# Kernel tuning notes

Hardware: AMD Instinct MI355X
Metric: run time of the kernel (lower is better)

Reference implementation:

```python
import jax, jax.numpy as jnp
import numpy as np
import math

NUM_CONVS = 4
GN_GROUPS = 32
GN_EPS = 1e-5
FPN_STRIDES = (8, 16, 32, 64, 128)
PRIOR_PROB = 0.01


def conv3x3(x, w, b):
    # x: [N,C,H,W], w: [O,I,3,3]
    y = jax.lax.conv_general_dilated(
        x, w, window_strides=(1, 1), padding='SAME',
        dimension_numbers=('NCHW', 'OIHW', 'NCHW'))
    return y + b[None, :, None, None]


def group_norm(x, gamma, beta):
    n, c, h, w = x.shape
    xg = x.reshape(n, GN_GROUPS, c // GN_GROUPS, h, w)
    mean = xg.mean(axis=(2, 3, 4), keepdims=True)
    var = xg.var(axis=(2, 3, 4), keepdims=True)
    xn = ((xg - mean) * jax.lax.rsqrt(var + GN_EPS)).reshape(n, c, h, w)
    return xn * gamma[None, :, None, None] + beta[None, :, None, None]


def subnet(x, ws, bs, gws, gbs):
    # NUM_CONVS x (conv3x3 -> GN -> ReLU)
    for i in range(NUM_CONVS):
        x = jax.nn.relu(group_norm(conv3x3(x, ws[i], bs[i]), gws[i], gbs[i]))
    return x


def permute_to_N_HWA_K(x, k):
    n = x.shape[0]
    return x.transpose(0, 2, 3, 1).reshape(n, -1, k)


def setup_inputs() -> dict:
    key = jax.random.key(0)
    ks = jax.random.split(key, 16)
    C, K = 256, 80
    feats = {
        'p3': jax.random.normal(ks[0], (1, C, 80, 80), jnp.float32),
        'p4': jax.random.normal(ks[1], (1, C, 40, 40), jnp.float32),
        'p5': jax.random.normal(ks[2], (1, C, 20, 20), jnp.float32),
        'p6': jax.random.normal(ks[3], (1, C, 10, 10), jnp.float32),
        'p7': jax.random.normal(ks[4], (1, C, 5, 5), jnp.float32),
    }
    std = 0.01
    bias_value = -math.log((1 - PRIOR_PROB) / PRIOR_PROB)
    params = {
        'cls_w': std * jax.random.normal(ks[5], (NUM_CONVS, C, C, 3, 3), jnp.float32),
        'cls_b': jnp.zeros((NUM_CONVS, C), jnp.float32),
        'cls_gn_w': jnp.ones((NUM_CONVS, C), jnp.float32),
        'cls_gn_b': jnp.zeros((NUM_CONVS, C), jnp.float32),
        'box_w': std * jax.random.normal(ks[6], (NUM_CONVS, C, C, 3, 3), jnp.float32),
        'box_b': jnp.zeros((NUM_CONVS, C), jnp.float32),
        'box_gn_w': jnp.ones((NUM_CONVS, C), jnp.float32),
        'box_gn_b': jnp.zeros((NUM_CONVS, C), jnp.float32),
        'score_w': std * jax.random.normal(ks[7], (K, C, 3, 3), jnp.float32),
        'score_b': jnp.full((K,), bias_value, jnp.float32),
        'pred_w': std * jax.random.normal(ks[8], (4, C, 3, 3), jnp.float32),
        'pred_b': jnp.zeros((4,), jnp.float32),
        'iou_w': std * jax.random.normal(ks[9], (1, C, 3, 3), jnp.float32),
        'iou_b': jnp.zeros((1,), jnp.float32),
        'scales': jnp.ones((5,), jnp.float32),
    }
    return {**feats, **params}


def reference(p3, p4, p5, p6, p7,
              cls_w, cls_b, cls_gn_w, cls_gn_b,
              box_w, box_b, box_gn_w, box_gn_b,
              score_w, score_b, pred_w, pred_b, iou_w, iou_b, scales):
    features = [p3, p4, p5, p6, p7]
    logits, bbox_reg, ious = [], [], []
    for l, feat in enumerate(features):
        c = subnet(feat, cls_w, cls_b, cls_gn_w, cls_gn_b)
        b = subnet(feat, box_w, box_b, box_gn_w, box_gn_b)
        logit = conv3x3(c, score_w, score_b)          # [N,80,H,W]
        iou = conv3x3(b, iou_w, iou_b)                # [N,1,H,W]
        bp = conv3x3(b, pred_w, pred_b) * scales[l]   # Scale module
        # norm_reg_targets=True branch
        reg = jax.nn.relu(bp) * FPN_STRIDES[l]        # [N,4,H,W]
        logits.append(permute_to_N_HWA_K(logit, 80))
        bbox_reg.append(permute_to_N_HWA_K(reg, 4))
        ious.append(permute_to_N_HWA_K(iou, 1))
    box_cls = jnp.concatenate(logits, axis=1)    # [N, sumHW, 80]
    box_delta = jnp.concatenate(bbox_reg, axis=1)  # [N, sumHW, 4]
    box_iou = jnp.concatenate(ious, axis=1)      # [N, sumHW, 1]
    # pack into one array for a single output: [N, sumHW, 85]
    return jnp.concatenate([box_cls, box_delta, box_iou], axis=-1)
```

## Files before the change

### kernel.cpp

```cpp
#include <hip/hip_runtime.h>

typedef unsigned short u16;
typedef __attribute__((ext_vector_type(8))) short bf16x8;
typedef __attribute__((ext_vector_type(4))) float f32x4;

#define NLEV 5
#define CCH 256
#define KTOT 2304
#define P_TOT 8525
#define PP_TOT 9165

__constant__ int   c_HW[NLEV]     = {6400, 1600, 400, 100, 25};
__constant__ int   c_W[NLEV]      = {80, 40, 20, 10, 5};
__constant__ int   c_off[NLEV]    = {0, 6400, 8000, 8400, 8500};
__constant__ int   c_poff[NLEV]   = {0, 6724, 8488, 8972, 9116};
__constant__ int   c_pts[NLEV+1]  = {0, 100, 125, 132, 134, 135};
__constant__ float c_stridef[NLEV]= {8.f, 16.f, 32.f, 64.f, 128.f};

__device__ __forceinline__ u16 f2bf(float f){
  union { float f; unsigned u; } v; v.f = f;
  unsigned r = v.u + 0x7fffu + ((v.u >> 16) & 1u);
  return (u16)(r >> 16);
}

__device__ __forceinline__ void g2l16(const u16* g, u16* l, int lane){
#if defined(__has_builtin)
#if __has_builtin(__builtin_amdgcn_global_load_lds)
  __builtin_amdgcn_global_load_lds(
      (const __attribute__((address_space(1))) unsigned int*)g,
      (__attribute__((address_space(3))) unsigned int*)l, 16, 0, 0);
  return;
#endif
#endif
  *(uint4*)(l + lane*8) = *(const uint4*)g;
}

template<int MODE>
__global__ __launch_bounds__(256) void gemm_conv(
    const u16* __restrict__ Xc, const u16* __restrict__ Xb,
    const u16* __restrict__ Wc, const u16* __restrict__ Wb,
    const float* __restrict__ bc, const float* __restrict__ bb,
    float* __restrict__ Yc, float* __restrict__ Yb,
    float* __restrict__ stats,
    const float* __restrict__ predb, const float* __restrict__ ioub,
    const float* __restrict__ scales, float* __restrict__ out)
{
  __shared__ u16 sA[128*32];
  __shared__ u16 sB[64*32];
  __shared__ float sstat[16][2];

  const int ptile = blockIdx.x, mtile = blockIdx.y, z = blockIdx.z;
  int lv = 0;
  #pragma unroll
  for (int i = 1; i < NLEV; i++) if (ptile >= c_pts[i]) lv = i;
  const int ptl = ptile - c_pts[lv];
  const int HW = c_HW[lv], Wl = c_W[lv];
  const int tid = threadIdx.x, wv = tid >> 6, ln = tid & 63;
  const int quad = ln >> 4, l15 = ln & 15;

  const u16* X  = z ? Xb : Xc;
  const u16* WA = z ? Wb : Wc;

  const int kl   = (ln & 3) * 8;
  const int rsub = ln >> 2;

  const u16* asrc0 = WA + (size_t)(mtile*128 + wv*32 + rsub) * KTOT + kl;
  const u16* asrc1 = asrc0 + (size_t)16 * KTOT;
  u16* adst0 = &sA[(wv*32)      * 32];
  u16* adst1 = &sA[(wv*32 + 16) * 32];

  const int prow = wv*16 + rsub;
  const int p = ptl*64 + prow;
  int pbase = 0;
  if (p < HW) { int h = p / Wl; int wi = p - h*Wl; pbase = h*(Wl+2) + wi; }
  const u16* bsrc = X + (size_t)(c_poff[lv] + pbase) * CCH + kl;
  u16* bdst = &sB[(wv*16) * 32];

  const u16* afp[2]; const u16* bfp[4];
  #pragma unroll
  for (int i = 0; i < 2; i++) afp[i] = &sA[((wv*32 + i*16 + l15) << 5) + quad*8];
  #pragma unroll
  for (int i = 0; i < 4; i++) bfp[i] = &sB[((i*16 + l15) << 5) + quad*8];

  f32x4 acc[2][4];
  #pragma unroll
  for (int i = 0; i < 2; i++)
    #pragma unroll
    for (int j = 0; j < 4; j++) acc[i][j] = (f32x4){0.f, 0.f, 0.f, 0.f};

  const int wrow = Wl + 2;
  for (int ch = 0; ch < 72; ch++) {
    const int tap = ch >> 3;
    const int dh = tap / 3, dw = tap - dh*3;
    const int aoff = ch * 32;
    const int boff = (dh*wrow + dw)*CCH + ((ch & 7) << 5);
    g2l16(asrc0 + aoff, adst0, ln);
    g2l16(asrc1 + aoff, adst1, ln);
    g2l16(bsrc + boff, bdst, ln);
    __syncthreads();
    bf16x8 af[2], bfr[4];
    #pragma unroll
    for (int i = 0; i < 2; i++) af[i]  = *(const bf16x8*)afp[i];
    #pragma unroll
    for (int i = 0; i < 4; i++) bfr[i] = *(const bf16x8*)bfp[i];
    #pragma unroll
    for (int i = 0; i < 2; i++)
      #pragma unroll
      for (int j = 0; j < 4; j++)
        acc[i][j] = __builtin_amdgcn_mfma_f32_16x16x32_bf16(af[i], bfr[j], acc[i][j], 0, 0, 0);
    __syncthreads();
  }

  const int nrem = HW - ptl*64;
  if (MODE == 0) {
    if (tid < 32) sstat[tid >> 1][tid & 1] = 0.f;
    __syncthreads();
    const float* bias = z ? bb : bc;
    float* Y = z ? Yb : Yc;
    #pragma unroll
    for (int mi = 0; mi < 2; mi++) {
      const int m0 = mtile*128 + wv*32 + mi*16 + quad*4;
      float s = 0.f, sq = 0.f;
      #pragma unroll
      for (int ni = 0; ni < 4; ni++) {
        const int nl = ni*16 + l15;
        f32x4 v = acc[mi][ni];
        #pragma unroll
        for (int r = 0; r < 4; r++) v[r] += bias[m0 + r];
        if (nl < nrem) {
          const size_t n = (size_t)(c_off[lv] + ptl*64 + nl);
          *(f32x4*)&Y[n*CCH + m0] = v;
          #pragma unroll
          for (int r = 0; r < 4; r++) { s += v[r]; sq += v[r]*v[r]; }
        }
      }
      #pragma unroll
      for (int o = 1; o < 16; o <<= 1) { s += __shfl_xor(s, o); sq += __shfl_xor(sq, o); }
      if (l15 == 0) {
        const int g = (wv*32 + mi*16 + quad*4) >> 3;
        atomicAdd(&sstat[g][0], s);
        atomicAdd(&sstat[g][1], sq);
      }
    }
    __syncthreads();
    if (tid < 32) {
      const int g = tid >> 1, c = tid & 1;
      atomicAdd(&stats[(((size_t)z*NLEV + lv)*32 + mtile*16 + g)*2 + c], sstat[g][c]);
    }
  } else {
    const float scl = scales[lv];
    const float stf = c_stridef[lv];
    #pragma unroll
    for (int mi = 0; mi < 2; mi++) {
      const int m0 = wv*32 + mi*16 + quad*4;
      if (m0 >= 85) continue;
      #pragma unroll
      for (int ni = 0; ni < 4; ni++) {
        const int nl = ni*16 + l15;
        if (nl >= nrem) continue;
        const size_t n = (size_t)(c_off[lv] + ptl*64 + nl);
        f32x4 v = acc[mi][ni];
        #pragma unroll
        for (int r = 0; r < 4; r++) {
          const int m = m0 + r;
          const float val = v[r];
          if (z == 0) {
            if (m < 80) out[n*85 + m] = val + bc[m];
          } else {
            if (m < 4) {
              const float t = (val + predb[m]) * scl;
              out[n*85 + 80 + m] = fmaxf(t, 0.f) * stf;
            } else if (m == 4) {
              out[n*85 + 84] = val + ioub[0];
            }
          }
        }
      }
    }
  }
}

__global__ __launch_bounds__(256) void gn_relu(
    const float* __restrict__ Yc, const float* __restrict__ Yb,
    const float* __restrict__ stats,
    const float* __restrict__ gwc, const float* __restrict__ gbc,
    const float* __restrict__ gwb, const float* __restrict__ gbb,
    u16* __restrict__ Xc, u16* __restrict__ Xb)
{
  const int t = blockIdx.x * 256 + threadIdx.x;
  if (t >= 2 * P_TOT * 32) return;
  const int br = t / (P_TOT * 32);
  const int r  = t - br * (P_TOT * 32);
  const int pg = r >> 5;
  const int c0 = (r & 31) << 3;
  int lv = 0;
  #pragma unroll
  for (int i = 1; i < NLEV; i++) if (pg >= c_off[i]) lv = i;
  const int pl = pg - c_off[lv];
  const int Wl = c_W[lv];
  const int g = c0 >> 3;
  const float* st = &stats[(((size_t)br*NLEV + lv)*32 + g)*2];
  const float cnt = 8.f * (float)c_HW[lv];
  const float mean = st[0] / cnt;
  const float var  = st[1] / cnt - mean*mean;
  const float rstd = rsqrtf(var + 1e-5f);
  const float* Y  = br ? Yb : Yc;
  const float* gw = br ? gwb : gwc;
  const float* gb = br ? gbb : gbc;
  u16* X = br ? Xb : Xc;
  const float* y = &Y[(size_t)pg*CCH + c0];
  const int h = pl / Wl, wi = pl - h*Wl;
  const size_t pidx = (size_t)(c_poff[lv] + (h+1)*(Wl+2) + (wi+1));
  union { u16 u[8]; uint4 v; } pk;
  #pragma unroll
  for (int i = 0; i < 8; i++) {
    const float v = (y[i] - mean)*rstd*gw[c0+i] + gb[c0+i];
    pk.u[i] = f2bf(fmaxf(v, 0.f));
  }
  *(uint4*)&X[pidx*CCH + c0] = pk.v;
}

__global__ __launch_bounds__(256) void feat2bf(
    const float* __restrict__ p3, const float* __restrict__ p4,
    const float* __restrict__ p5, const float* __restrict__ p6,
    const float* __restrict__ p7, u16* __restrict__ X)
{
  const int t = blockIdx.x * 256 + threadIdx.x;
  if (t >= P_TOT * 32) return;
  const int pg = t >> 5, c0 = (t & 31) << 3;
  int lv = 0;
  #pragma unroll
  for (int i = 1; i < NLEV; i++) if (pg >= c_off[i]) lv = i;
  const int pl = pg - c_off[lv];
  const float* src = lv==0 ? p3 : lv==1 ? p4 : lv==2 ? p5 : lv==3 ? p6 : p7;
  const int HW = c_HW[lv], Wl = c_W[lv];
  const int h = pl / Wl, wi = pl - h*Wl;
  const size_t pidx = (size_t)(c_poff[lv] + (h+1)*(Wl+2) + (wi+1));
  union { u16 u[8]; uint4 v; } pk;
  #pragma unroll
  for (int i = 0; i < 8; i++)
    pk.u[i] = f2bf(src[(size_t)(c0+i)*HW + pl]);
  *(uint4*)&X[pidx*CCH + c0] = pk.v;
}

__global__ __launch_bounds__(256) void wconv(
    const float* __restrict__ cw, const float* __restrict__ bw,
    u16* __restrict__ Wc, u16* __restrict__ Wb)
{
  const size_t N = (size_t)4*256*KTOT;
  const size_t t = (size_t)blockIdx.x * 256 + threadIdx.x;
  if (t >= 2*N) return;
  const float* src = (t < N) ? cw : bw;
  u16* dst = (t < N) ? Wc : Wb;
  const size_t i = (t < N) ? t : t - N;
  const size_t lc = i / KTOT;
  const int kk = (int)(i - lc*KTOT);
  const int tap = kk >> 8, ci = kk & 255;
  dst[i] = f2bf(src[(lc*256 + ci)*9 + tap]);
}

__global__ __launch_bounds__(256) void hconv(
    const float* __restrict__ sw, const float* __restrict__ pw,
    const float* __restrict__ iw, u16* __restrict__ Whc, u16* __restrict__ Whb)
{
  const int N = 128 * KTOT;
  const int t = blockIdx.x * 256 + threadIdx.x;
  if (t >= 2*N) return;
  const int i = (t < N) ? t : t - N;
  const int co = i / KTOT, kk = i - co*KTOT;
  const int tap = kk >> 8, ci = kk & 255;
  float v = 0.f;
  if (t < N) {
    if (co < 80) v = sw[(co*256 + ci)*9 + tap];
    Whc[i] = f2bf(v);
  } else {
    if (co < 4)       v = pw[(co*256 + ci)*9 + tap];
    else if (co == 4) v = iw[ci*9 + tap];
    Whb[i] = f2bf(v);
  }
}

extern "C" void kernel_launch(void* const* d_in, const int* in_sizes, int n_in,
                              void* d_out, int out_size, void* d_ws, size_t ws_size,
                              hipStream_t stream)
{
  const float* p3      = (const float*)d_in[0];
  const float* p4      = (const float*)d_in[1];
  const float* p5      = (const float*)d_in[2];
  const float* p6      = (const float*)d_in[3];
  const float* p7      = (const float*)d_in[4];
  const float* cls_w   = (const float*)d_in[5];
  const float* cls_b   = (const float*)d_in[6];
  const float* cls_gw  = (const float*)d_in[7];
  const float* cls_gb  = (const float*)d_in[8];
  const float* box_w   = (const float*)d_in[9];
  const float* box_b   = (const float*)d_in[10];
  const float* box_gw  = (const float*)d_in[11];
  const float* box_gb  = (const float*)d_in[12];
  const float* score_w = (const float*)d_in[13];
  const float* score_b = (const float*)d_in[14];
  const float* pred_w  = (const float*)d_in[15];
  const float* pred_b  = (const float*)d_in[16];
  const float* iou_w   = (const float*)d_in[17];
  const float* iou_b   = (const float*)d_in[18];
  const float* scales  = (const float*)d_in[19];
  float* out = (float*)d_out;

  char* w = (char*)d_ws;
  size_t o = 0;
  auto alloc = [&](size_t b) { void* p = w + o; o += (b + 255) & ~(size_t)255; return p; };
  u16* WRC = (u16*)alloc((size_t)4*256*KTOT*2);
  u16* WRB = (u16*)alloc((size_t)4*256*KTOT*2);
  u16* WHC = (u16*)alloc((size_t)128*KTOT*2);
  u16* WHB = (u16*)alloc((size_t)128*KTOT*2);
  u16* XF  = (u16*)alloc((size_t)PP_TOT*CCH*2);
  u16* XC0 = (u16*)alloc((size_t)PP_TOT*CCH*2);
  u16* XC1 = (u16*)alloc((size_t)PP_TOT*CCH*2);
  u16* XB0 = (u16*)alloc((size_t)PP_TOT*CCH*2);
  u16* XB1 = (u16*)alloc((size_t)PP_TOT*CCH*2);
  float* YC = (float*)alloc((size_t)P_TOT*CCH*4);
  float* YB = (float*)alloc((size_t)P_TOT*CCH*4);
  float* ST = (float*)alloc((size_t)2*5*32*2*4);

  hipMemsetAsync(XF, 0, (size_t)5*PP_TOT*CCH*2, stream);
  hipMemsetAsync(ST, 0, (size_t)2*5*32*2*4, stream);

  wconv<<<dim3((unsigned)(((size_t)2*4*256*KTOT + 255)/256)), 256, 0, stream>>>(cls_w, box_w, WRC, WRB);
  hconv<<<dim3((2*128*KTOT + 255)/256), 256, 0, stream>>>(score_w, pred_w, iou_w, WHC, WHB);
  feat2bf<<<dim3((P_TOT*32 + 255)/256), 256, 0, stream>>>(p3, p4, p5, p6, p7, XF);

  const u16* xci = XF; const u16* xbi = XF;
  u16* xcs[4] = {XC0, XC1, XC0, XC1};
  u16* xbs[4] = {XB0, XB1, XB0, XB1};
  for (int l = 0; l < 4; l++) {
    gemm_conv<0><<<dim3(135, 2, 2), 256, 0, stream>>>(
        xci, xbi, WRC + (size_t)l*256*KTOT, WRB + (size_t)l*256*KTOT,
        cls_b + l*256, box_b + l*256, YC, YB, ST,
        nullptr, nullptr, nullptr, nullptr);
    gn_relu<<<dim3((2*P_TOT*32 + 255)/256), 256, 0, stream>>>(
        YC, YB, ST, cls_gw + l*256, cls_gb + l*256, box_gw + l*256, box_gb + l*256,
        xcs[l], xbs[l]);
    if (l < 3) hipMemsetAsync(ST, 0, (size_t)2*5*32*2*4, stream);
    xci = xcs[l]; xbi = xbs[l];
  }
  gemm_conv<1><<<dim3(135, 1, 2), 256, 0, stream>>>(
      xci, xbi, WHC, WHB, score_b, nullptr, nullptr, nullptr, nullptr,
      pred_b, iou_b, scales, out);
}
```

Baseline: 408.4 us.

## Split conv GEMM K across blocks with 64-wide swizzled LDS tiles and separate GN stats

Each conv GEMM now splits the 2304-long K dimension into two halves across extra grid z-slices. Each slice writes its own fp32 partial output buffer. The K step per iteration grows from 32 to 64, with an XOR swizzle on LDS rows to avoid bank conflicts. Bias addition and GroupNorm statistics move out of the GEMM epilogue into a new gn_stats kernel that sums the partials, and the head epilogue moves into a head_out kernel. The goal is more blocks in flight and fewer barriers per K element, paid for by extra partial-buffer traffic and more kernel launches per layer.

Measured after the change: 452.3 us. 1.11x slower.

```diff
diff --git a/kernel.cpp b/kernel.cpp
--- a/kernel.cpp
+++ b/kernel.cpp
@@ -36,51 +36,43 @@
 }
 
 template<int MODE>
-__global__ __launch_bounds__(256) void gemm_conv(
+__global__ __launch_bounds__(256, 4) void gemm_conv(
     const u16* __restrict__ Xc, const u16* __restrict__ Xb,
     const u16* __restrict__ Wc, const u16* __restrict__ Wb,
-    const float* __restrict__ bc, const float* __restrict__ bb,
-    float* __restrict__ Yc, float* __restrict__ Yb,
-    float* __restrict__ stats,
-    const float* __restrict__ predb, const float* __restrict__ ioub,
-    const float* __restrict__ scales, float* __restrict__ out)
-{
-  __shared__ u16 sA[128*32];
-  __shared__ u16 sB[64*32];
-  __shared__ float sstat[16][2];
-
-  const int ptile = blockIdx.x, mtile = blockIdx.y, z = blockIdx.z;
+    float* __restrict__ Y0c, float* __restrict__ Y1c,
+    float* __restrict__ Y0b, float* __restrict__ Y1b,
+    float* __restrict__ OP)
+{
+  __shared__ u16 sA[128*64];
+  __shared__ u16 sB[64*64];
+
+  const int ptile = blockIdx.x, mtile = blockIdx.y;
+  const int kh = blockIdx.z >> 1, br = blockIdx.z & 1;
   int lv = 0;
   #pragma unroll
   for (int i = 1; i < NLEV; i++) if (ptile >= c_pts[i]) lv = i;
   const int ptl = ptile - c_pts[lv];
-  const int HW = c_HW[lv], Wl = c_W[lv];
+  const int HW = c_HW[lv], Wl = c_W[lv], wrow = Wl + 2;
   const int tid = threadIdx.x, wv = tid >> 6, ln = tid & 63;
   const int quad = ln >> 4, l15 = ln & 15;
-
-  const u16* X  = z ? Xb : Xc;
-  const u16* WA = z ? Wb : Wc;
-
-  const int kl   = (ln & 3) * 8;
-  const int rsub = ln >> 2;
-
-  const u16* asrc0 = WA + (size_t)(mtile*128 + wv*32 + rsub) * KTOT + kl;
-  const u16* asrc1 = asrc0 + (size_t)16 * KTOT;
-  u16* adst0 = &sA[(wv*32)      * 32];
-  u16* adst1 = &sA[(wv*32 + 16) * 32];
-
-  const int prow = wv*16 + rsub;
-  const int p = ptl*64 + prow;
-  int pbase = 0;
-  if (p < HW) { int h = p / Wl; int wi = p - h*Wl; pbase = h*(Wl+2) + wi; }
-  const u16* bsrc = X + (size_t)(c_poff[lv] + pbase) * CCH + kl;
-  u16* bdst = &sB[(wv*16) * 32];
-
-  const u16* afp[2]; const u16* bfp[4];
-  #pragma unroll
-  for (int i = 0; i < 2; i++) afp[i] = &sA[((wv*32 + i*16 + l15) << 5) + quad*8];
-  #pragma unroll
-  for (int i = 0; i < 4; i++) bfp[i] = &sB[((i*16 + l15) << 5) + quad*8];
+  const int lr = ln >> 3;
+  const int gsw = (ln & 7) ^ lr;
+
+  const u16* X  = br ? Xb : Xc;
+  const u16* WA = br ? Wb : Wc;
+
+  const u16* abase = WA + (size_t)(mtile*128 + wv*32 + lr) * KTOT + gsw*8;
+  u16* adst = &sA[(wv*32) * 64];
+
+  const u16* bptr[2];
+  #pragma unroll
+  for (int j = 0; j < 2; j++) {
+    const int p = ptl*64 + wv*16 + j*8 + lr;
+    int pb = 0;
+    if (p < HW) { int h = p / Wl; int wi = p - h*Wl; pb = h*wrow + wi; }
+    bptr[j] = X + (size_t)(c_poff[lv] + pb) * CCH + gsw*8;
+  }
+  u16* bdst = &sB[(wv*16) * 64];
 
   f32x4 acc[2][4];
   #pragma unroll
@@ -88,101 +80,112 @@
     #pragma unroll
     for (int j = 0; j < 4; j++) acc[i][j] = (f32x4){0.f, 0.f, 0.f, 0.f};
 
-  const int wrow = Wl + 2;
-  for (int ch = 0; ch < 72; ch++) {
-    const int tap = ch >> 3;
+  const int s0 = kh * 18, s1 = s0 + 18;
+  for (int s = s0; s < s1; s++) {
+    const int tap = s >> 2;
     const int dh = tap / 3, dw = tap - dh*3;
-    const int aoff = ch * 32;
-    const int boff = (dh*wrow + dw)*CCH + ((ch & 7) << 5);
-    g2l16(asrc0 + aoff, adst0, ln);
-    g2l16(asrc1 + aoff, adst1, ln);
-    g2l16(bsrc + boff, bdst, ln);
+    const u16* as = abase + (size_t)s * 64;
+    g2l16(as,            adst,         ln);
+    g2l16(as +  8*KTOT,  adst +  8*64, ln);
+    g2l16(as + 16*KTOT,  adst + 16*64, ln);
+    g2l16(as + 24*KTOT,  adst + 24*64, ln);
+    const int bsh = (dh*wrow + dw)*CCH + ((s & 3) << 6);
+    g2l16(bptr[0] + bsh, bdst,         ln);
+    g2l16(bptr[1] + bsh, bdst +  8*64, ln);
     __syncthreads();
-    bf16x8 af[2], bfr[4];
-    #pragma unroll
-    for (int i = 0; i < 2; i++) af[i]  = *(const bf16x8*)afp[i];
-    #pragma unroll
-    for (int i = 0; i < 4; i++) bfr[i] = *(const bf16x8*)bfp[i];
-    #pragma unroll
-    for (int i = 0; i < 2; i++)
+    bf16x8 af[2][2], bf[2][4];
+    #pragma unroll
+    for (int sub = 0; sub < 2; sub++) {
+      const int gbase = (sub*4 + quad) ^ (l15 & 7);
+      #pragma unroll
+      for (int i = 0; i < 2; i++)
+        af[sub][i] = *(const bf16x8*)&sA[(wv*32 + i*16 + l15)*64 + gbase*8];
       #pragma unroll
       for (int j = 0; j < 4; j++)
-        acc[i][j] = __builtin_amdgcn_mfma_f32_16x16x32_bf16(af[i], bfr[j], acc[i][j], 0, 0, 0);
+        bf[sub][j] = *(const bf16x8*)&sB[(j*16 + l15)*64 + gbase*8];
+    }
+    #pragma unroll
+    for (int sub = 0; sub < 2; sub++)
+      #pragma unroll
+      for (int i = 0; i < 2; i++)
+        #pragma unroll
+        for (int j = 0; j < 4; j++)
+          acc[i][j] = __builtin_amdgcn_mfma_f32_16x16x32_bf16(af[sub][i], bf[sub][j], acc[i][j], 0, 0, 0);
     __syncthreads();
   }
 
   const int nrem = HW - ptl*64;
   if (MODE == 0) {
-    if (tid < 32) sstat[tid >> 1][tid & 1] = 0.f;
-    __syncthreads();
-    const float* bias = z ? bb : bc;
-    float* Y = z ? Yb : Yc;
+    float* Y = br ? (kh ? Y1b : Y0b) : (kh ? Y1c : Y0c);
     #pragma unroll
     for (int mi = 0; mi < 2; mi++) {
       const int m0 = mtile*128 + wv*32 + mi*16 + quad*4;
-      float s = 0.f, sq = 0.f;
       #pragma unroll
       for (int ni = 0; ni < 4; ni++) {
         const int nl = ni*16 + l15;
-        f32x4 v = acc[mi][ni];
-        #pragma unroll
-        for (int r = 0; r < 4; r++) v[r] += bias[m0 + r];
         if (nl < nrem) {
           const size_t n = (size_t)(c_off[lv] + ptl*64 + nl);
-          *(f32x4*)&Y[n*CCH + m0] = v;
-          #pragma unroll
-          for (int r = 0; r < 4; r++) { s += v[r]; sq += v[r]*v[r]; }
-        }
-      }
-      #pragma unroll
-      for (int o = 1; o < 16; o <<= 1) { s += __shfl_xor(s, o); sq += __shfl_xor(sq, o); }
-      if (l15 == 0) {
-        const int g = (wv*32 + mi*16 + quad*4) >> 3;
-        atomicAdd(&sstat[g][0], s);
-        atomicAdd(&sstat[g][1], sq);
-      }
-    }
-    __syncthreads();
-    if (tid < 32) {
-      const int g = tid >> 1, c = tid & 1;
-      atomicAdd(&stats[(((size_t)z*NLEV + lv)*32 + mtile*16 + g)*2 + c], sstat[g][c]);
-    }
-  } else {
-    const float scl = scales[lv];
-    const float stf = c_stridef[lv];
-    #pragma unroll
-    for (int mi = 0; mi < 2; mi++) {
-      const int m0 = wv*32 + mi*16 + quad*4;
-      if (m0 >= 85) continue;
-      #pragma unroll
-      for (int ni = 0; ni < 4; ni++) {
-        const int nl = ni*16 + l15;
-        if (nl >= nrem) continue;
-        const size_t n = (size_t)(c_off[lv] + ptl*64 + nl);
-        f32x4 v = acc[mi][ni];
-        #pragma unroll
-        for (int r = 0; r < 4; r++) {
-          const int m = m0 + r;
-          const float val = v[r];
-          if (z == 0) {
-            if (m < 80) out[n*85 + m] = val + bc[m];
-          } else {
-            if (m < 4) {
-              const float t = (val + predb[m]) * scl;
-              out[n*85 + 80 + m] = fmaxf(t, 0.f) * stf;
-            } else if (m == 4) {
-              out[n*85 + 84] = val + ioub[0];
-            }
-          }
+          *(f32x4*)&Y[n*CCH + m0] = acc[mi][ni];
         }
       }
     }
+  } else {
+    float* O = OP + (size_t)(br*2 + kh) * P_TOT * 128;
+    #pragma unroll
+    for (int mi = 0; mi < 2; mi++) {
+      const int m0 = wv*32 + mi*16 + quad*4;
+      #pragma unroll
+      for (int ni = 0; ni < 4; ni++) {
+        const int nl = ni*16 + l15;
+        if (nl < nrem) {
+          const size_t n = (size_t)(c_off[lv] + ptl*64 + nl);
+          *(f32x4*)&O[n*128 + m0] = acc[mi][ni];
+        }
+      }
+    }
+  }
+}
+
+__global__ __launch_bounds__(256) void gn_stats(
+    const float* __restrict__ Y0c, const float* __restrict__ Y1c,
+    const float* __restrict__ Y0b, const float* __restrict__ Y1b,
+    const float* __restrict__ bc, const float* __restrict__ bb,
+    float* __restrict__ stats)
+{
+  const int sl = blockIdx.x, br = blockIdx.y;
+  int lv = 0;
+  #pragma unroll
+  for (int i = 1; i < NLEV; i++) if (sl >= c_pts[i]) lv = i;
+  const int sll = sl - c_pts[lv];
+  const int HW = c_HW[lv];
+  const float* Y0 = br ? Y0b : Y0c;
+  const float* Y1 = br ? Y1b : Y1c;
+  const int c = threadIdx.x;
+  const float b = (br ? bb : bc)[c];
+  float s = 0.f, sq = 0.f;
+  const int p0 = sll * 64;
+  for (int i = 0; i < 64; i++) {
+    const int p = p0 + i;
+    if (p >= HW) break;
+    const size_t idx = (size_t)(c_off[lv] + p) * CCH + c;
+    const float v = Y0[idx] + Y1[idx] + b;
+    s += v; sq += v*v;
+  }
+  s += __shfl_xor(s, 1); sq += __shfl_xor(sq, 1);
+  s += __shfl_xor(s, 2); sq += __shfl_xor(sq, 2);
+  s += __shfl_xor(s, 4); sq += __shfl_xor(sq, 4);
+  if ((c & 7) == 0) {
+    const int g = c >> 3;
+    atomicAdd(&stats[((br*NLEV + lv)*32 + g)*2 + 0], s);
+    atomicAdd(&stats[((br*NLEV + lv)*32 + g)*2 + 1], sq);
   }
 }
 
 __global__ __launch_bounds__(256) void gn_relu(
-    const float* __restrict__ Yc, const float* __restrict__ Yb,
+    const float* __restrict__ Y0c, const float* __restrict__ Y1c,
+    const float* __restrict__ Y0b, const float* __restrict__ Y1b,
     const float* __restrict__ stats,
+    const float* __restrict__ bc, const float* __restrict__ bb,
     const float* __restrict__ gwc, const float* __restrict__ gbc,
     const float* __restrict__ gwb, const float* __restrict__ gbb,
     u16* __restrict__ Xc, u16* __restrict__ Xb)
@@ -204,20 +207,49 @@
   const float mean = st[0] / cnt;
   const float var  = st[1] / cnt - mean*mean;
   const float rstd = rsqrtf(var + 1e-5f);
-  const float* Y  = br ? Yb : Yc;
+  const float* Y0 = br ? Y0b : Y0c;
+  const float* Y1 = br ? Y1b : Y1c;
+  const float* bs = br ? bb : bc;
   const float* gw = br ? gwb : gwc;
   const float* gb = br ? gbb : gbc;
   u16* X = br ? Xb : Xc;
-  const float* y = &Y[(size_t)pg*CCH + c0];
+  const float* y0 = &Y0[(size_t)pg*CCH + c0];
+  const float* y1 = &Y1[(size_t)pg*CCH + c0];
   const int h = pl / Wl, wi = pl - h*Wl;
   const size_t pidx = (size_t)(c_poff[lv] + (h+1)*(Wl+2) + (wi+1));
   union { u16 u[8]; uint4 v; } pk;
   #pragma unroll
   for (int i = 0; i < 8; i++) {
-    const float v = (y[i] - mean)*rstd*gw[c0+i] + gb[c0+i];
+    const float v = (y0[i] + y1[i] + bs[c0+i] - mean)*rstd*gw[c0+i] + gb[c0+i];
     pk.u[i] = f2bf(fmaxf(v, 0.f));
   }
   *(uint4*)&X[pidx*CCH + c0] = pk.v;
+}
+
+__global__ __launch_bounds__(256) void head_out(
+    const float* __restrict__ OP,
+    const float* __restrict__ score_b, const float* __restrict__ pred_b,
+    const float* __restrict__ iou_b, const float* __restrict__ scales,
+    float* __restrict__ out)
+{
+  const int t = blockIdx.x * 256 + threadIdx.x;
+  if (t >= P_TOT * 96) return;
+  const int n = t / 96, m = t - n*96;
+  if (m >= 85) return;
+  int lv = 0;
+  #pragma unroll
+  for (int i = 1; i < NLEV; i++) if (n >= c_off[i]) lv = i;
+  const size_t S = (size_t)P_TOT * 128;
+  const size_t r = (size_t)n * 128;
+  if (m < 80) {
+    out[(size_t)n*85 + m] = OP[r + m] + OP[S + r + m] + score_b[m];
+  } else if (m < 84) {
+    const int mm = m - 80;
+    float v = (OP[2*S + r + mm] + OP[3*S + r + mm] + pred_b[mm]) * scales[lv];
+    out[(size_t)n*85 + 80 + mm] = fmaxf(v, 0.f) * c_stridef[lv];
+  } else {
+    out[(size_t)n*85 + 84] = OP[2*S + r + 4] + OP[3*S + r + 4] + iou_b[0];
+  }
 }
 
 __global__ __launch_bounds__(256) void feat2bf(
@@ -314,36 +346,37 @@
   u16* WHC = (u16*)alloc((size_t)128*KTOT*2);
   u16* WHB = (u16*)alloc((size_t)128*KTOT*2);
   u16* XF  = (u16*)alloc((size_t)PP_TOT*CCH*2);
-  u16* XC0 = (u16*)alloc((size_t)PP_TOT*CCH*2);
-  u16* XC1 = (u16*)alloc((size_t)PP_TOT*CCH*2);
-  u16* XB0 = (u16*)alloc((size_t)PP_TOT*CCH*2);
-  u16* XB1 = (u16*)alloc((size_t)PP_TOT*CCH*2);
-  float* YC = (float*)alloc((size_t)P_TOT*CCH*4);
-  float* YB = (float*)alloc((size_t)P_TOT*CCH*4);
-  float* ST = (float*)alloc((size_t)2*5*32*2*4);
-
-  hipMemsetAsync(XF, 0, (size_t)5*PP_TOT*CCH*2, stream);
-  hipMemsetAsync(ST, 0, (size_t)2*5*32*2*4, stream);
+  u16* XC  = (u16*)alloc((size_t)PP_TOT*CCH*2);
+  u16* XB  = (u16*)alloc((size_t)PP_TOT*CCH*2);
+  float* Y0C = (float*)alloc((size_t)P_TOT*CCH*4);
+  float* Y1C = (float*)alloc((size_t)P_TOT*CCH*4);
+  float* Y0B = (float*)alloc((size_t)P_TOT*CCH*4);
+  float* Y1B = (float*)alloc((size_t)P_TOT*CCH*4);
+  float* OP  = (float*)alloc((size_t)4*P_TOT*128*4);
+  float* ST  = (float*)alloc((size_t)2*NLEV*32*2*4);
+
+  hipMemsetAsync(XF, 0, (size_t)3*PP_TOT*CCH*2, stream);
 
   wconv<<<dim3((unsigned)(((size_t)2*4*256*KTOT + 255)/256)), 256, 0, stream>>>(cls_w, box_w, WRC, WRB);
   hconv<<<dim3((2*128*KTOT + 255)/256), 256, 0, stream>>>(score_w, pred_w, iou_w, WHC, WHB);
   feat2bf<<<dim3((P_TOT*32 + 255)/256), 256, 0, stream>>>(p3, p4, p5, p6, p7, XF);
 
   const u16* xci = XF; const u16* xbi = XF;
-  u16* xcs[4] = {XC0, XC1, XC0, XC1};
-  u16* xbs[4] = {XB0, XB1, XB0, XB1};
   for (int l = 0; l < 4; l++) {
-    gemm_conv<0><<<dim3(135, 2, 2), 256, 0, stream>>>(
+    hipMemsetAsync(ST, 0, (size_t)2*NLEV*32*2*4, stream);
+    gemm_conv<0><<<dim3(135, 2, 4), 256, 0, stream>>>(
         xci, xbi, WRC + (size_t)l*256*KTOT, WRB + (size_t)l*256*KTOT,
-        cls_b + l*256, box_b + l*256, YC, YB, ST,
-        nullptr, nullptr, nullptr, nullptr);
+        Y0C, Y1C, Y0B, Y1B, nullptr);
+    gn_stats<<<dim3(135, 2), 256, 0, stream>>>(
+        Y0C, Y1C, Y0B, Y1B, cls_b + l*256, box_b + l*256, ST);
     gn_relu<<<dim3((2*P_TOT*32 + 255)/256), 256, 0, stream>>>(
-        YC, YB, ST, cls_gw + l*256, cls_gb + l*256, box_gw + l*256, box_gb + l*256,
-        xcs[l], xbs[l]);
-    if (l < 3) hipMemsetAsync(ST, 0, (size_t)2*5*32*2*4, stream);
-    xci = xcs[l]; xbi = xbs[l];
-  }
-  gemm_conv<1><<<dim3(135, 1, 2), 256, 0, stream>>>(
-      xci, xbi, WHC, WHB, score_b, nullptr, nullptr, nullptr, nullptr,
-      pred_b, iou_b, scales, out);
-}
+        Y0C, Y1C, Y0B, Y1B, ST, cls_b + l*256, box_b + l*256,
+        cls_gw + l*256, cls_gb + l*256, box_gw + l*256, box_gb + l*256,
+        XC, XB);
+    xci = XC; xbi = XB;
+  }
+  gemm_conv<1><<<dim3(135, 1, 4), 256, 0, stream>>>(
+      xci, xbi, WHC, WHB, nullptr, nullptr, nullptr, nullptr, OP);
+  head_out<<<dim3((P_TOT*96 + 255)/256), 256, 0, stream>>>(
+      OP, score_b, pred_b, iou_b, scales, out);
+}
```

## Replace LDS-staged conv GEMM with register double-buffered 64x64 wave tiles

Applied to the files above, without the earlier changes.

The implicit-GEMM conv kernel no longer stages A and B tiles through LDS with two barriers per K step. Each wave now loads MFMA fragments straight from global memory into registers, double-buffered across K steps, and computes a 64x64 output tile. For the trunk convs this makes each block cover all 256 output channels, so the grid is halved. The head kernel is remapped so each wave owns one pixel tile and the box branch launches only one channel tile. Activation buffers are single-buffered, and GN stats get a slice per layer that is cleared by one up-front memset instead of memsets between layers. The trade-off is less shared-memory reuse, heavier reliance on L1/L2 for fragment loads, more registers, and fewer resident waves per CU.

Result: slower. 779.1 us (+90.7%).

```diff
diff --git a/kernel.cpp b/kernel.cpp
--- a/kernel.cpp
+++ b/kernel.cpp
@@ -15,24 +15,13 @@
 __constant__ int   c_off[NLEV]    = {0, 6400, 8000, 8400, 8500};
 __constant__ int   c_poff[NLEV]   = {0, 6724, 8488, 8972, 9116};
 __constant__ int   c_pts[NLEV+1]  = {0, 100, 125, 132, 134, 135};
+__constant__ int   c_g4s[NLEV+1]  = {0, 25, 32, 34, 35, 36};
 __constant__ float c_stridef[NLEV]= {8.f, 16.f, 32.f, 64.f, 128.f};
 
 __device__ __forceinline__ u16 f2bf(float f){
   union { float f; unsigned u; } v; v.f = f;
   unsigned r = v.u + 0x7fffu + ((v.u >> 16) & 1u);
   return (u16)(r >> 16);
-}
-
-__device__ __forceinline__ void g2l16(const u16* g, u16* l, int lane){
-#if defined(__has_builtin)
-#if __has_builtin(__builtin_amdgcn_global_load_lds)
-  __builtin_amdgcn_global_load_lds(
-      (const __attribute__((address_space(1))) unsigned int*)g,
-      (__attribute__((address_space(3))) unsigned int*)l, 16, 0, 0);
-  return;
-#endif
-#endif
-  *(uint4*)(l + lane*8) = *(const uint4*)g;
 }
 
 template<int MODE>
@@ -45,91 +34,102 @@
     const float* __restrict__ predb, const float* __restrict__ ioub,
     const float* __restrict__ scales, float* __restrict__ out)
 {
-  __shared__ u16 sA[128*32];
-  __shared__ u16 sB[64*32];
-  __shared__ float sstat[16][2];
-
-  const int ptile = blockIdx.x, mtile = blockIdx.y, z = blockIdx.z;
-  int lv = 0;
-  #pragma unroll
-  for (int i = 1; i < NLEV; i++) if (ptile >= c_pts[i]) lv = i;
-  const int ptl = ptile - c_pts[lv];
-  const int HW = c_HW[lv], Wl = c_W[lv];
+  __shared__ float sstat[32][2];
   const int tid = threadIdx.x, wv = tid >> 6, ln = tid & 63;
   const int quad = ln >> 4, l15 = ln & 15;
 
-  const u16* X  = z ? Xb : Xc;
-  const u16* WA = z ? Wb : Wc;
-
-  const int kl   = (ln & 3) * 8;
-  const int rsub = ln >> 2;
-
-  const u16* asrc0 = WA + (size_t)(mtile*128 + wv*32 + rsub) * KTOT + kl;
-  const u16* asrc1 = asrc0 + (size_t)16 * KTOT;
-  u16* adst0 = &sA[(wv*32)      * 32];
-  u16* adst1 = &sA[(wv*32 + 16) * 32];
-
-  const int prow = wv*16 + rsub;
-  const int p = ptl*64 + prow;
-  int pbase = 0;
-  if (p < HW) { int h = p / Wl; int wi = p - h*Wl; pbase = h*(Wl+2) + wi; }
-  const u16* bsrc = X + (size_t)(c_poff[lv] + pbase) * CCH + kl;
-  u16* bdst = &sB[(wv*16) * 32];
-
-  const u16* afp[2]; const u16* bfp[4];
-  #pragma unroll
-  for (int i = 0; i < 2; i++) afp[i] = &sA[((wv*32 + i*16 + l15) << 5) + quad*8];
-  #pragma unroll
-  for (int i = 0; i < 4; i++) bfp[i] = &sB[((i*16 + l15) << 5) + quad*8];
-
-  f32x4 acc[2][4];
-  #pragma unroll
-  for (int i = 0; i < 2; i++)
+  int lv = 0, ptl, m0, br;
+  if (MODE == 0) {
+    const int ptile = blockIdx.x;
+    br = blockIdx.z;
+    #pragma unroll
+    for (int i = 1; i < NLEV; i++) if (ptile >= c_pts[i]) lv = i;
+    ptl = ptile - c_pts[lv];
+    m0 = wv * 64;
+  } else {
+    const int gx = blockIdx.x, gy = blockIdx.y;
+    br = (gy == 2) ? 1 : 0;
+    m0 = (gy == 1) ? 64 : 0;
+    #pragma unroll
+    for (int i = 1; i < NLEV; i++) if (gx >= c_g4s[i]) lv = i;
+    ptl = (gx - c_g4s[lv]) * 4 + wv;
+    if (ptl >= c_pts[lv+1] - c_pts[lv]) return;
+  }
+  const int HW = c_HW[lv], Wl = c_W[lv], wrow = Wl + 2;
+  const u16* __restrict__ X  = br ? Xb : Xc;
+  const u16* __restrict__ WA = br ? Wb : Wc;
+
+  int ar[4], rb[4];
+  #pragma unroll
+  for (int mt = 0; mt < 4; mt++) ar[mt] = (m0 + mt*16 + l15) * KTOT + quad*8;
+  #pragma unroll
+  for (int nt = 0; nt < 4; nt++) {
+    const int p = ptl*64 + nt*16 + l15;
+    int rbase = wrow + 1;
+    if (p < HW) { const int h = p / Wl, wi = p - h*Wl; rbase = (h+1)*wrow + (wi+1); }
+    rb[nt] = (c_poff[lv] + rbase) * CCH + quad*8;
+  }
+
+  f32x4 acc[4][4];
+  #pragma unroll
+  for (int i = 0; i < 4; i++)
     #pragma unroll
     for (int j = 0; j < 4; j++) acc[i][j] = (f32x4){0.f, 0.f, 0.f, 0.f};
 
-  const int wrow = Wl + 2;
-  for (int ch = 0; ch < 72; ch++) {
-    const int tap = ch >> 3;
-    const int dh = tap / 3, dw = tap - dh*3;
-    const int aoff = ch * 32;
-    const int boff = (dh*wrow + dw)*CCH + ((ch & 7) << 5);
-    g2l16(asrc0 + aoff, adst0, ln);
-    g2l16(asrc1 + aoff, adst1, ln);
-    g2l16(bsrc + boff, bdst, ln);
-    __syncthreads();
-    bf16x8 af[2], bfr[4];
-    #pragma unroll
-    for (int i = 0; i < 2; i++) af[i]  = *(const bf16x8*)afp[i];
-    #pragma unroll
-    for (int i = 0; i < 4; i++) bfr[i] = *(const bf16x8*)bfp[i];
-    #pragma unroll
-    for (int i = 0; i < 2; i++)
-      #pragma unroll
-      for (int j = 0; j < 4; j++)
-        acc[i][j] = __builtin_amdgcn_mfma_f32_16x16x32_bf16(af[i], bfr[j], acc[i][j], 0, 0, 0);
-    __syncthreads();
-  }
+  bf16x8 A0[4], B0[4], A1[4], B1[4];
+
+#define LDFRAG(Af, Bf, S) do {                                              \
+    const int _s = (S);                                                     \
+    const int _tap = _s >> 3;                                               \
+    const int _dh = _tap / 3, _dw = _tap - _dh*3;                           \
+    const int _aof = _s * 32;                                               \
+    const int _bof = ((_dh-1)*wrow + (_dw-1))*CCH + ((_s & 7) << 5);        \
+    _Pragma("unroll")                                                       \
+    for (int _mt = 0; _mt < 4; _mt++)                                       \
+      Af[_mt] = *(const bf16x8*)(WA + ar[_mt] + _aof);                      \
+    _Pragma("unroll")                                                       \
+    for (int _nt = 0; _nt < 4; _nt++)                                       \
+      Bf[_nt] = *(const bf16x8*)(X + rb[_nt] + _bof);                       \
+  } while (0)
+
+#define MFMA16(Af, Bf) do {                                                 \
+    _Pragma("unroll")                                                       \
+    for (int _mt = 0; _mt < 4; _mt++)                                       \
+      _Pragma("unroll")                                                     \
+      for (int _nt = 0; _nt < 4; _nt++)                                     \
+        acc[_mt][_nt] = __builtin_amdgcn_mfma_f32_16x16x32_bf16(            \
+            Af[_mt], Bf[_nt], acc[_mt][_nt], 0, 0, 0);                      \
+  } while (0)
+
+  LDFRAG(A0, B0, 0);
+  for (int s = 0; s < 72; s += 2) {
+    LDFRAG(A1, B1, s + 1);
+    MFMA16(A0, B0);
+    const int s2 = (s + 2 < 72) ? s + 2 : 70;
+    LDFRAG(A0, B0, s2);
+    MFMA16(A1, B1);
+  }
+#undef LDFRAG
+#undef MFMA16
 
   const int nrem = HW - ptl*64;
   if (MODE == 0) {
-    if (tid < 32) sstat[tid >> 1][tid & 1] = 0.f;
+    if (tid < 64) sstat[tid >> 1][tid & 1] = 0.f;
     __syncthreads();
-    const float* bias = z ? bb : bc;
-    float* Y = z ? Yb : Yc;
-    #pragma unroll
-    for (int mi = 0; mi < 2; mi++) {
-      const int m0 = mtile*128 + wv*32 + mi*16 + quad*4;
+    const float* __restrict__ bias = br ? bb : bc;
+    float* __restrict__ Y = br ? Yb : Yc;
+    #pragma unroll
+    for (int mt = 0; mt < 4; mt++) {
+      const int mrow = m0 + mt*16 + quad*4;
+      const f32x4 bv = *(const f32x4*)&bias[mrow];
       float s = 0.f, sq = 0.f;
       #pragma unroll
-      for (int ni = 0; ni < 4; ni++) {
-        const int nl = ni*16 + l15;
-        f32x4 v = acc[mi][ni];
-        #pragma unroll
-        for (int r = 0; r < 4; r++) v[r] += bias[m0 + r];
+      for (int nt = 0; nt < 4; nt++) {
+        const int nl = nt*16 + l15;
+        f32x4 v = acc[mt][nt] + bv;
         if (nl < nrem) {
           const size_t n = (size_t)(c_off[lv] + ptl*64 + nl);
-          *(f32x4*)&Y[n*CCH + m0] = v;
+          *(f32x4*)&Y[n*CCH + mrow] = v;
           #pragma unroll
           for (int r = 0; r < 4; r++) { s += v[r]; sq += v[r]*v[r]; }
         }
@@ -137,41 +137,39 @@
       #pragma unroll
       for (int o = 1; o < 16; o <<= 1) { s += __shfl_xor(s, o); sq += __shfl_xor(sq, o); }
       if (l15 == 0) {
-        const int g = (wv*32 + mi*16 + quad*4) >> 3;
+        const int g = mrow >> 3;
         atomicAdd(&sstat[g][0], s);
         atomicAdd(&sstat[g][1], sq);
       }
     }
     __syncthreads();
-    if (tid < 32) {
+    if (tid < 64) {
       const int g = tid >> 1, c = tid & 1;
-      atomicAdd(&stats[(((size_t)z*NLEV + lv)*32 + mtile*16 + g)*2 + c], sstat[g][c]);
+      atomicAdd(&stats[((br*NLEV + lv)*32 + g)*2 + c], sstat[g][c]);
     }
   } else {
     const float scl = scales[lv];
     const float stf = c_stridef[lv];
     #pragma unroll
-    for (int mi = 0; mi < 2; mi++) {
-      const int m0 = wv*32 + mi*16 + quad*4;
-      if (m0 >= 85) continue;
+    for (int mt = 0; mt < 4; mt++) {
+      const int mr0 = m0 + mt*16 + quad*4;
       #pragma unroll
-      for (int ni = 0; ni < 4; ni++) {
-        const int nl = ni*16 + l15;
+      for (int nt = 0; nt < 4; nt++) {
+        const int nl = nt*16 + l15;
         if (nl >= nrem) continue;
         const size_t n = (size_t)(c_off[lv] + ptl*64 + nl);
-        f32x4 v = acc[mi][ni];
+        const f32x4 v = acc[mt][nt];
         #pragma unroll
         for (int r = 0; r < 4; r++) {
-          const int m = m0 + r;
-          const float val = v[r];
-          if (z == 0) {
-            if (m < 80) out[n*85 + m] = val + bc[m];
+          const int m = mr0 + r;
+          if (br == 0) {
+            if (m < 80) out[n*85 + m] = v[r] + bc[m];
           } else {
             if (m < 4) {
-              const float t = (val + predb[m]) * scl;
+              const float t = (v[r] + predb[m]) * scl;
               out[n*85 + 80 + m] = fmaxf(t, 0.f) * stf;
             } else if (m == 4) {
-              out[n*85 + 84] = val + ioub[0];
+              out[n*85 + 84] = v[r] + ioub[0];
             }
           }
         }
@@ -309,41 +307,36 @@
   char* w = (char*)d_ws;
   size_t o = 0;
   auto alloc = [&](size_t b) { void* p = w + o; o += (b + 255) & ~(size_t)255; return p; };
-  u16* WRC = (u16*)alloc((size_t)4*256*KTOT*2);
-  u16* WRB = (u16*)alloc((size_t)4*256*KTOT*2);
-  u16* WHC = (u16*)alloc((size_t)128*KTOT*2);
-  u16* WHB = (u16*)alloc((size_t)128*KTOT*2);
-  u16* XF  = (u16*)alloc((size_t)PP_TOT*CCH*2);
-  u16* XC0 = (u16*)alloc((size_t)PP_TOT*CCH*2);
-  u16* XC1 = (u16*)alloc((size_t)PP_TOT*CCH*2);
-  u16* XB0 = (u16*)alloc((size_t)PP_TOT*CCH*2);
-  u16* XB1 = (u16*)alloc((size_t)PP_TOT*CCH*2);
+  u16*   XF = (u16*)alloc((size_t)PP_TOT*CCH*2);
+  u16*   XC = (u16*)alloc((size_t)PP_TOT*CCH*2);
+  u16*   XB = (u16*)alloc((size_t)PP_TOT*CCH*2);
+  float* ST = (float*)alloc((size_t)4*2*NLEV*32*2*4);
+  u16*  WRC = (u16*)alloc((size_t)4*256*KTOT*2);
+  u16*  WRB = (u16*)alloc((size_t)4*256*KTOT*2);
+  u16*  WHC = (u16*)alloc((size_t)128*KTOT*2);
+  u16*  WHB = (u16*)alloc((size_t)128*KTOT*2);
   float* YC = (float*)alloc((size_t)P_TOT*CCH*4);
   float* YB = (float*)alloc((size_t)P_TOT*CCH*4);
-  float* ST = (float*)alloc((size_t)2*5*32*2*4);
-
-  hipMemsetAsync(XF, 0, (size_t)5*PP_TOT*CCH*2, stream);
-  hipMemsetAsync(ST, 0, (size_t)2*5*32*2*4, stream);
+
+  hipMemsetAsync(XF, 0, (size_t)3*PP_TOT*CCH*2 + (size_t)4*2*NLEV*32*2*4, stream);
 
   wconv<<<dim3((unsigned)(((size_t)2*4*256*KTOT + 255)/256)), 256, 0, stream>>>(cls_w, box_w, WRC, WRB);
   hconv<<<dim3((2*128*KTOT + 255)/256), 256, 0, stream>>>(score_w, pred_w, iou_w, WHC, WHB);
   feat2bf<<<dim3((P_TOT*32 + 255)/256), 256, 0, stream>>>(p3, p4, p5, p6, p7, XF);
 
   const u16* xci = XF; const u16* xbi = XF;
-  u16* xcs[4] = {XC0, XC1, XC0, XC1};
-  u16* xbs[4] = {XB0, XB1, XB0, XB1};
   for (int l = 0; l < 4; l++) {
-    gemm_conv<0><<<dim3(135, 2, 2), 256, 0, stream>>>(
+    float* STl = ST + (size_t)l*2*NLEV*32*2;
+    gemm_conv<0><<<dim3(135, 1, 2), 256, 0, stream>>>(
         xci, xbi, WRC + (size_t)l*256*KTOT, WRB + (size_t)l*256*KTOT,
-        cls_b + l*256, box_b + l*256, YC, YB, ST,
+        cls_b + l*256, box_b + l*256, YC, YB, STl,
         nullptr, nullptr, nullptr, nullptr);
     gn_relu<<<dim3((2*P_TOT*32 + 255)/256), 256, 0, stream>>>(
-        YC, YB, ST, cls_gw + l*256, cls_gb + l*256, box_gw + l*256, box_gb + l*256,
-        xcs[l], xbs[l]);
-    if (l < 3) hipMemsetAsync(ST, 0, (size_t)2*5*32*2*4, stream);
-    xci = xcs[l]; xbi = xbs[l];
-  }
-  gemm_conv<1><<<dim3(135, 1, 2), 256, 0, stream>>>(
+        YC, YB, STl, cls_gw + l*256, cls_gb + l*256, box_gw + l*256, box_gb + l*256,
+        XC, XB);
+    xci = XC; xbi = XB;
+  }
+  gemm_conv<1><<<dim3(36, 3, 1), 256, 0, stream>>>(
       xci, xbi, WHC, WHB, score_b, nullptr, nullptr, nullptr, nullptr,
       pred_b, iou_b, scales, out);
 }
```
